# Kernel optimization log

Measured on AMD Instinct MI355X. Metric: run time of the kernel, lower is better.

## Reference

```python
import jax, jax.numpy as jnp
import numpy as np

Nc, Nq = 100000, 20000
Fc, Fq = 300, 768
HID, H, L = 128, 4, 2
D = HID // H
OUT = 8
E = 400000
NT, ET = 2, 3


def setup_inputs() -> dict:
    key = jax.random.key(0)
    ks = jax.random.split(key, 24)
    def n(i, shape, s=1.0):
        return jax.random.normal(ks[i], shape, dtype=jnp.float32) * s
    return {
        'x_context': n(0, (Nc, Fc)),
        'x_question': n(1, (Nq, Fq)),
        'src_q2c': jax.random.randint(ks[2], (E,), 0, Nq),
        'dst_q2c': jax.random.randint(ks[3], (E,), 0, Nc),
        'src_c2c': jax.random.randint(ks[4], (E,), 0, Nc),
        'dst_c2c': jax.random.randint(ks[5], (E,), 0, Nc),
        'src_c2q': jax.random.randint(ks[6], (E,), 0, Nc),
        'dst_c2q': jax.random.randint(ks[7], (E,), 0, Nq),
        'in_W_context': n(8, (Fc, HID), 0.05),
        'in_b_context': jnp.zeros((HID,), jnp.float32),
        'in_W_question': n(9, (Fq, HID), 0.05),
        'in_b_question': jnp.zeros((HID,), jnp.float32),
        'k_W': n(10, (L, NT, HID, HID), 0.05),
        'k_b': jnp.zeros((L, NT, HID), jnp.float32),
        'q_W': n(11, (L, NT, HID, HID), 0.05),
        'q_b': jnp.zeros((L, NT, HID), jnp.float32),
        'v_W': n(12, (L, NT, HID, HID), 0.05),
        'v_b': jnp.zeros((L, NT, HID), jnp.float32),
        'a_W': n(13, (L, NT, HID, HID), 0.05),
        'a_b': jnp.zeros((L, NT, HID), jnp.float32),
        'skip': jnp.ones((L, NT), jnp.float32),
        'a_rel': n(14, (L, ET, H, D, D), 0.1),
        'm_rel': n(15, (L, ET, H, D, D), 0.1),
        'p_rel': jnp.ones((L, ET, H), jnp.float32),
        'out_W': n(16, (HID, OUT), 0.05),
        'out_b': jnp.zeros((OUT,), jnp.float32),
    }


def segment_softmax(logits, seg, num):
    # logits: [E, H], seg: [E] destination node ids
    m = jax.ops.segment_max(logits, seg, num_segments=num)
    m = jnp.where(jnp.isfinite(m), m, 0.0)
    e = jnp.exp(logits - m[seg])
    s = jax.ops.segment_sum(e, seg, num_segments=num)
    return e / (s[seg] + 1e-16)


def reference(x_context, x_question, src_q2c, dst_q2c, src_c2c, dst_c2c,
              src_c2q, dst_c2q, in_W_context, in_b_context, in_W_question,
              in_b_question, k_W, k_b, q_W, q_b, v_W, v_b, a_W, a_b, skip,
              a_rel, m_rel, p_rel, out_W, out_b):
    # node type 0 = 'context', 1 = 'question'
    x = [jax.nn.relu(x_context @ in_W_context + in_b_context),
         jax.nn.relu(x_question @ in_W_question + in_b_question)]
    Ns = [x[0].shape[0], x[1].shape[0]]
    # (src_nt, dst_nt, src_idx, dst_idx) per edge type
    edge_types = [(1, 0, src_q2c, dst_q2c),
                  (0, 0, src_c2c, dst_c2c),
                  (0, 1, src_c2q, dst_c2q)]
    scale = 1.0 / jnp.sqrt(jnp.float32(D))
    for l in range(L):
        k = [(x[nt] @ k_W[l, nt] + k_b[l, nt]).reshape(-1, H, D) for nt in range(NT)]
        q = [(x[nt] @ q_W[l, nt] + q_b[l, nt]).reshape(-1, H, D) for nt in range(NT)]
        v = [(x[nt] @ v_W[l, nt] + v_b[l, nt]).reshape(-1, H, D) for nt in range(NT)]
        agg = [jnp.zeros((Ns[nt], H, D), x[0].dtype) for nt in range(NT)]
        for et, (snt, dnt, src, dst) in enumerate(edge_types):
            k_rel = jnp.einsum('ehd,hdf->ehf', k[snt][src], a_rel[l, et])
            v_rel = jnp.einsum('ehd,hdf->ehf', v[snt][src], m_rel[l, et])
            logits = jnp.einsum('ehd,ehd->eh', q[dnt][dst], k_rel) * p_rel[l, et] * scale
            alpha = segment_softmax(logits, dst, Ns[dnt])  # [E, H]
            agg[dnt] = agg[dnt].at[dst].add(v_rel * alpha[:, :, None])
        for nt in range(NT):
            o = jax.nn.gelu(agg[nt].reshape(Ns[nt], HID), approximate=False)
            o = o @ a_W[l, nt] + a_b[l, nt]
            g = jax.nn.sigmoid(skip[l, nt])
            x[nt] = g * o + (1.0 - g) * x[nt]
    return x[0] @ out_W + out_b
```

## Files before the change

kernel.cpp:

```cpp
#include <hip/hip_runtime.h>

constexpr int NC = 100000;
constexpr int NQ = 20000;
constexpr int FC = 300;
constexpr int FQ = 768;
constexpr int NEDGE = 400000;
constexpr int NTOT = NC + NC + NQ;
constexpr int NTOT2 = NC + NQ;
constexpr int NB0 = (NC + 127) / 128;
constexpr int NB1 = (NQ + 127) / 128;
constexpr int NBALL = NB0 + NB1;
constexpr int NBC64 = (NC + 63) / 64;
constexpr int NBQ64 = (NQ + 63) / 64;
constexpr int NBALL64 = NBC64 + NBQ64;
constexpr float SCALE = 0.17677669529663687f;
constexpr float LOG2E = 1.4426950408889634f;

typedef __attribute__((ext_vector_type(8))) short bf16x8;
typedef __attribute__((ext_vector_type(4))) float f32x4;
typedef unsigned short u16;

__device__ __forceinline__ float gelu_f(float x) {
  return 0.5f * x * (1.0f + erff(x * 0.7071067811865476f));
}
__device__ __forceinline__ u16 bf16_rne(float x) {
  unsigned u = __float_as_uint(x);
  unsigned r = u + 0x7fffu + ((u >> 16) & 1u);
  return (u16)(r >> 16);
}
__device__ __forceinline__ float bf16_to_f(u16 h) {
  return __uint_as_float(((unsigned)h) << 16);
}
__device__ __forceinline__ void split2(float x, u16& hi, u16& lo) {
  hi = bf16_rne(x);
  lo = bf16_rne(x - bf16_to_f(hi));
}
__device__ __forceinline__ void splitT(float x, u16& hi, u16& lo) {
  hi = (u16)(__float_as_uint(x) >> 16);
  lo = bf16_rne(x - bf16_to_f(hi));
}

__global__ void k_count3(const int* __restrict__ d0, const int* __restrict__ d1,
                         const int* __restrict__ d2, int* __restrict__ counts) {
  int i = blockIdx.x * 256 + threadIdx.x;
  if (i >= 3 * NEDGE) return;
  int et = i / NEDGE, e = i - et * NEDGE;
  int d = (et == 0) ? d0[e] : (et == 1) ? d1[e] : d2[e];
  int base = (et == 0) ? 0 : (et == 1) ? NC : 2 * NC;
  atomicAdd(&counts[base + d], 1);
}

__global__ void k_scan_block(const int* __restrict__ in, int* __restrict__ out,
                             int* __restrict__ bsum, int n) {
  __shared__ int s[256];
  int tid = threadIdx.x;
  int i = blockIdx.x * 256 + tid;
  int v = (i < n) ? in[i] : 0;
  s[tid] = v;
  __syncthreads();
  for (int off = 1; off < 256; off <<= 1) {
    int t = (tid >= off) ? s[tid - off] : 0;
    __syncthreads();
    s[tid] += t;
    __syncthreads();
  }
  if (i < n) out[i] = s[tid] - v;
  if (tid == 255) bsum[blockIdx.x] = s[255];
}

__global__ void k_scan_sums(int* __restrict__ bsum, int nb) {
  __shared__ int s[1024];
  int tid = threadIdx.x;
  int v = (tid < nb) ? bsum[tid] : 0;
  s[tid] = v;
  __syncthreads();
  for (int off = 1; off < 1024; off <<= 1) {
    int t = (tid >= off) ? s[tid - off] : 0;
    __syncthreads();
    s[tid] += t;
    __syncthreads();
  }
  if (tid < nb) bsum[tid] = s[tid] - v;
}

__global__ void k_scan_add(int* __restrict__ ptr, const int* __restrict__ bsum,
                           int* __restrict__ cursor, int n, int total) {
  int i = blockIdx.x * 256 + threadIdx.x;
  if (i < n) {
    int v = ptr[i] + bsum[blockIdx.x];
    ptr[i] = v;
    cursor[i] = v;
  }
  if (i == 0) ptr[n] = total;
}

__global__ void k_scatter3(const int* __restrict__ s0, const int* __restrict__ s1,
                           const int* __restrict__ s2, const int* __restrict__ d0,
                           const int* __restrict__ d1, const int* __restrict__ d2,
                           int* __restrict__ cursor, int* __restrict__ srcs_out) {
  int i = blockIdx.x * 256 + threadIdx.x;
  if (i >= 3 * NEDGE) return;
  int et = i / NEDGE, e = i - et * NEDGE;
  int d = (et == 0) ? d0[e] : (et == 1) ? d1[e] : d2[e];
  int sv = (et == 0) ? s0[e] : (et == 1) ? s1[e] : s2[e];
  int base = (et == 0) ? 0 : (et == 1) ? NC : 2 * NC;
  int p = atomicAdd(&cursor[base + d], 1);
  srcs_out[p] = sv;
}

__global__ void prep_all(const float* __restrict__ kW, const float* __restrict__ kB,
                         const float* __restrict__ qW, const float* __restrict__ qB,
                         const float* __restrict__ vW, const float* __restrict__ vB,
                         const float* __restrict__ aW, const float* __restrict__ aB,
                         const float* __restrict__ arel, const float* __restrict__ mrel,
                         const float* __restrict__ prel,
                         u16* __restrict__ Bth, u16* __restrict__ Btl,
                         float* __restrict__ biasOut) {
  int i = blockIdx.x;
  int col = threadIdx.x;
  int y = blockIdx.y;
  int l = y / 10, yy = y % 10;
  size_t lw = (size_t)l * 2 * 16384, lb = (size_t)l * 2 * 128;
  size_t le = (size_t)l * 3 * 4096, lp = (size_t)l * 3 * 4;
  const float *W = nullptr, *bb = nullptr, *rel = nullptr, *pr = nullptr;
  float mscale = 1.0f;
  bool fold = false;
  switch (yy) {
    case 0: W = qW + lw; bb = qB + lb; break;
    case 1: fold = true; W = kW + lw; bb = kB + lb; rel = arel + le + 4096; pr = prel + lp + 4; mscale = SCALE; break;
    case 2: fold = true; W = vW + lw; bb = vB + lb; rel = mrel + le + 4096; break;
    case 3: fold = true; W = kW + lw; bb = kB + lb; rel = arel + le + 8192; pr = prel + lp + 8; mscale = SCALE; break;
    case 4: fold = true; W = vW + lw; bb = vB + lb; rel = mrel + le + 8192; break;
    case 5: W = qW + lw + 16384; bb = qB + lb + 128; break;
    case 6: fold = true; W = kW + lw + 16384; bb = kB + lb + 128; rel = arel + le; pr = prel + lp; mscale = SCALE; break;
    case 7: fold = true; W = vW + lw + 16384; bb = vB + lb + 128; rel = mrel + le; break;
    case 8: W = aW + lw; bb = aB + lb; break;
    default: W = aW + lw + 16384; bb = aB + lb + 128; break;
  }
  int colOff = y * 128;
  if (!fold) {
    float v = W[i * 128 + col];
    u16 hi, lo;
    split2(v, hi, lo);
    Bth[(size_t)(colOff + col) * 128 + i] = hi;
    Btl[(size_t)(colOff + col) * 128 + i] = lo;
    if (i == 0) biasOut[colOff + col] = bb[col];
    return;
  }
  int h = col >> 5, f = col & 31;
  float m = (pr ? pr[h] : 1.0f) * mscale;
  float s = 0.0f;
  #pragma unroll
  for (int d = 0; d < 32; ++d)
    s += W[i * 128 + h * 32 + d] * rel[(h * 32 + d) * 32 + f];
  s *= m;
  u16 hi, lo;
  split2(s, hi, lo);
  Bth[(size_t)(colOff + col) * 128 + i] = hi;
  Btl[(size_t)(colOff + col) * 128 + i] = lo;
  if (i == 0) {
    float sb = 0.0f;
    #pragma unroll
    for (int d = 0; d < 32; ++d)
      sb += bb[h * 32 + d] * rel[(h * 32 + d) * 32 + f];
    biasOut[colOff + col] = sb * m;
  }
}

__global__ void split_in(const float* __restrict__ Wc, const float* __restrict__ bc,
                         const float* __restrict__ Wq, const float* __restrict__ bq,
                         u16* __restrict__ Bth, u16* __restrict__ Btl,
                         float* __restrict__ biasOut) {
  int n = blockIdx.x, y = blockIdx.y;
  const float* W = y ? Wq : Wc;
  const float* b = y ? bq : bc;
  int K = y ? FQ : FC, Kp = y ? 768 : 320;
  size_t boff = y ? (size_t)128 * 320 : 0;
  for (int k = threadIdx.x; k < Kp; k += 256) {
    float v = (k < K) ? W[(size_t)k * 128 + n] : 0.0f;
    u16 hi, lo;
    split2(v, hi, lo);
    Bth[boff + (size_t)n * Kp + k] = hi;
    Btl[boff + (size_t)n * Kp + k] = lo;
  }
  if (threadIdx.x == 0) biasOut[(y ? 128 : 0) + n] = b[n];
}

template <int MODE>
__global__ __launch_bounds__(256) void pipe_gemm(
    const float* __restrict__ Ac, const float* __restrict__ Aq,
    const u16* __restrict__ Bth, const u16* __restrict__ Btl,
    const float* __restrict__ biasBuf,
    u16* __restrict__ xh_all, u16* __restrict__ xl_all,
    const float* __restrict__ skip, int l) {
  __shared__ u16 smem[15360];
  constexpr int AH = 0, AL = 2560, BH = 5120, BL = 10240;
  const int tid = threadIdx.x, lane = tid & 63, wv = tid >> 6;
  const int l15 = lane & 15, g4 = lane >> 4, koff = g4 * 8;
  const int srA = tid >> 2, scA = (tid & 3) * 8;
  const int srB = tid >> 1, scB = (tid & 1) * 16;

  const int bid = blockIdx.x;
  const int nt = (bid < NBC64) ? 0 : 1;
  const int m0 = nt ? (bid - NBC64) * 64 : bid * 64;
  const int M = nt ? NQ : NC;
  const int rowbase = nt ? NC : 0;
  const float* A32;
  int K, Kp, biasOff;
  size_t boff, arow;
  if (MODE == 1) {
    if (nt == 0) { A32 = Ac; K = FC; Kp = 320; boff = 0; biasOff = 0; }
    else { A32 = Aq; K = FQ; Kp = 768; boff = (size_t)128 * 320; biasOff = 128; }
    arow = (size_t)(m0 + srA) * K;
  } else {
    A32 = Ac;
    K = 128; Kp = 128;
    boff = (size_t)(8 + nt) * 16384;
    biasOff = (8 + nt) * 128;
    arow = (size_t)(rowbase + m0 + srA) * 128;
  }
  const bool rowokA = (m0 + srA) < M;
  const int nk = (K + 31) / 32;

  f32x4 acc[8];
  #pragma unroll
  for (int ni = 0; ni < 8; ++ni) acc[ni] = (f32x4){0.f, 0.f, 0.f, 0.f};

  auto loadA = [&](float va[8], int k0) {
    if (rowokA && (k0 + 32 <= K)) {
      const float* ap = A32 + arow + k0 + scA;
      float4 f0 = *(const float4*)ap;
      float4 f1 = *(const float4*)(ap + 4);
      va[0] = f0.x; va[1] = f0.y; va[2] = f0.z; va[3] = f0.w;
      va[4] = f1.x; va[5] = f1.y; va[6] = f1.z; va[7] = f1.w;
    } else {
      #pragma unroll
      for (int j = 0; j < 8; ++j) {
        int kc = k0 + scA + j;
        va[j] = (rowokA && kc < K) ? A32[arow + kc] : 0.0f;
      }
    }
  };
  auto loadB = [&](uint4& bh0, uint4& bh1, uint4& bl0, uint4& bl1, int k0) {
    const u16* bp = Bth + boff + (size_t)srB * Kp + k0 + scB;
    bh0 = *(const uint4*)bp;
    bh1 = *(const uint4*)(bp + 8);
    const u16* lp = Btl + boff + (size_t)srB * Kp + k0 + scB;
    bl0 = *(const uint4*)lp;
    bl1 = *(const uint4*)(lp + 8);
  };

  float vaC[8];
  uint4 bhC0, bhC1, blC0, blC1;
  loadA(vaC, 0);
  loadB(bhC0, bhC1, blC0, blC1, 0);

  for (int ks = 0; ks < nk; ++ks) {
    {
      alignas(16) u16 hv[8], lv[8];
      #pragma unroll
      for (int j = 0; j < 8; ++j) {
        float x = (MODE == 2) ? gelu_f(vaC[j]) : vaC[j];
        splitT(x, hv[j], lv[j]);
      }
      *(uint4*)&smem[AH + srA * 40 + scA] = *(const uint4*)hv;
      *(uint4*)&smem[AL + srA * 40 + scA] = *(const uint4*)lv;
      *(uint4*)&smem[BH + srB * 40 + scB] = bhC0;
      *(uint4*)&smem[BH + srB * 40 + scB + 8] = bhC1;
      *(uint4*)&smem[BL + srB * 40 + scB] = blC0;
      *(uint4*)&smem[BL + srB * 40 + scB + 8] = blC1;
    }
    __syncthreads();

    float vaN[8];
    uint4 bhN0, bhN1, blN0, blN1;
    const bool more = (ks + 1) < nk;
    if (more) {
      loadA(vaN, (ks + 1) * 32);
      loadB(bhN0, bhN1, blN0, blN1, (ks + 1) * 32);
    }

    {
      int row = wv * 16 + l15;
      bf16x8 a_h = *(const bf16x8*)&smem[AH + row * 40 + koff];
      bf16x8 a_l = *(const bf16x8*)&smem[AL + row * 40 + koff];
      #pragma unroll
      for (int ni = 0; ni < 8; ++ni) {
        int col = ni * 16 + l15;
        bf16x8 b_h = *(const bf16x8*)&smem[BH + col * 40 + koff];
        bf16x8 b_l = *(const bf16x8*)&smem[BL + col * 40 + koff];
        acc[ni] = __builtin_amdgcn_mfma_f32_16x16x32_bf16(a_h, b_h, acc[ni], 0, 0, 0);
        acc[ni] = __builtin_amdgcn_mfma_f32_16x16x32_bf16(a_l, b_h, acc[ni], 0, 0, 0);
        acc[ni] = __builtin_amdgcn_mfma_f32_16x16x32_bf16(a_h, b_l, acc[ni], 0, 0, 0);
      }
    }
    __syncthreads();

    if (more) {
      #pragma unroll
      for (int j = 0; j < 8; ++j) vaC[j] = vaN[j];
      bhC0 = bhN0; bhC1 = bhN1; blC0 = blN0; blC1 = blN1;
    }
  }

  float g = 1.0f;
  if (MODE == 2) g = 1.0f / (1.0f + __expf(-skip[l * 2 + nt]));

  const int rl0 = wv * 16 + g4 * 4;
  #pragma unroll
  for (int ni = 0; ni < 8; ++ni) {
    int colL = ni * 16 + l15;
    float bi = biasBuf[biasOff + colL];
    #pragma unroll
    for (int rr = 0; rr < 4; ++rr) {
      int row = m0 + rl0 + rr;
      float o = acc[ni][rr] + bi;
      if (MODE == 1) {
        o = fmaxf(o, 0.0f);
      } else if (row < M) {
        size_t idx = (size_t)(rowbase + row) * 128 + colL;
        float xo = bf16_to_f(xh_all[idx]) + bf16_to_f(xl_all[idx]);
        o = g * o + (1.0f - g) * xo;
      }
      acc[ni][rr] = o;
    }
  }

  const int wrow = tid >> 2, wseg = tid & 3;
  #pragma unroll
  for (int ph = 0; ph < 2; ++ph) {
    if (ph) __syncthreads();
    #pragma unroll
    for (int ni = 0; ni < 8; ++ni) {
      #pragma unroll
      for (int rr = 0; rr < 4; ++rr) {
        u16 hh, ll;
        split2(acc[ni][rr], hh, ll);
        smem[(rl0 + rr) * 136 + ni * 16 + l15] = ph ? ll : hh;
      }
    }
    __syncthreads();
    int grow = m0 + wrow;
    if (grow < M) {
      u16* dstp = ph ? xl_all : xh_all;
      uint4* dst = (uint4*)&dstp[(size_t)(rowbase + grow) * 128 + wseg * 32];
      const uint4* src = (const uint4*)&smem[wrow * 136 + wseg * 32];
      #pragma unroll
      for (int j = 0; j < 4; ++j) dst[j] = src[j];
    }
  }
}

__global__ __launch_bounds__(256) void proj_all(
    const u16* __restrict__ xh_all,
    const u16* __restrict__ Bth, const float* __restrict__ biasBuf,
    u16* __restrict__ q_all, u16* __restrict__ kvA,
    u16* __restrict__ kvB1, u16* __restrict__ kvB2) {
  int bid = blockIdx.x, y = blockIdx.y;
  int nt = (bid < NB0) ? 0 : 1;
  if (nt == 1 && y >= 3) return;
  __shared__ u16 smem[10240];
  constexpr int AH = 0, BH = 5120;
  int m0 = nt ? (bid - NB0) * 128 : bid * 128;
  int M = nt ? NQ : NC;
  int abase = nt ? NC : 0;
  int bslab = nt ? 5 + y : y;
  u16* cp; int ld, cb, crowbase;
  if (nt == 0) {
    switch (y) {
      case 0: cp = q_all; ld = 128; cb = 0; crowbase = 0; break;
      case 1: cp = kvB1; ld = 256; cb = 0; crowbase = 0; break;
      case 2: cp = kvB1; ld = 256; cb = 128; crowbase = 0; break;
      case 3: cp = kvB2; ld = 256; cb = 0; crowbase = 0; break;
      default: cp = kvB2; ld = 256; cb = 128; crowbase = 0; break;
    }
  } else {
    switch (y) {
      case 0: cp = q_all; ld = 128; cb = 0; crowbase = NC; break;
      case 1: cp = kvA; ld = 256; cb = 0; crowbase = 0; break;
      default: cp = kvA; ld = 256; cb = 128; crowbase = 0; break;
    }
  }
  const int tid = threadIdx.x, lane = tid & 63, wv = tid >> 6;
  const int l15 = lane & 15, g4 = lane >> 4, koff = g4 * 8;
  const int sr = tid >> 1, sc = (tid & 1) * 16;
  const bool rowok = (m0 + sr) < M;

  f32x4 acc[2][8];
  #pragma unroll
  for (int mi = 0; mi < 2; ++mi)
    #pragma unroll
    for (int ni = 0; ni < 8; ++ni) acc[mi][ni] = (f32x4){0.f, 0.f, 0.f, 0.f};

  for (int k0 = 0; k0 < 128; k0 += 32) {
    uint4 h0 = {0, 0, 0, 0}, h1 = {0, 0, 0, 0};
    if (rowok) {
      const u16* ap = xh_all + (size_t)(abase + m0 + sr) * 128 + k0 + sc;
      h0 = *(const uint4*)ap;
      h1 = *(const uint4*)(ap + 8);
    }
    *(uint4*)&smem[AH + sr * 40 + sc] = h0;
    *(uint4*)&smem[AH + sr * 40 + sc + 8] = h1;
    {
      const u16* bp = Bth + (size_t)(bslab * 128 + sr) * 128 + k0 + sc;
      *(uint4*)&smem[BH + sr * 40 + sc] = *(const uint4*)bp;
      *(uint4*)&smem[BH + sr * 40 + sc + 8] = *(const uint4*)(bp + 8);
    }
    __syncthreads();

    bf16x8 a_h[2];
    #pragma unroll
    for (int mi = 0; mi < 2; ++mi) {
      int row = wv * 32 + mi * 16 + l15;
      a_h[mi] = *(const bf16x8*)&smem[AH + row * 40 + koff];
    }
    #pragma unroll
    for (int ni = 0; ni < 8; ++ni) {
      int col = ni * 16 + l15;
      bf16x8 b_h = *(const bf16x8*)&smem[BH + col * 40 + koff];
      #pragma unroll
      for (int mi = 0; mi < 2; ++mi)
        acc[mi][ni] = __builtin_amdgcn_mfma_f32_16x16x32_bf16(a_h[mi], b_h, acc[mi][ni], 0, 0, 0);
    }
    __syncthreads();
  }

  const int wrow = tid >> 2, wseg = tid & 3;
  #pragma unroll
  for (int h = 0; h < 2; ++h) {
    if (h) __syncthreads();
    if ((wv >> 1) == h) {
      #pragma unroll
      for (int mi = 0; mi < 2; ++mi) {
        int rl = (wv & 1) * 32 + mi * 16 + g4 * 4;
        #pragma unroll
        for (int ni = 0; ni < 8; ++ni) {
          float bi = biasBuf[bslab * 128 + ni * 16 + l15];
          #pragma unroll
          for (int rr = 0; rr < 4; ++rr)
            smem[(rl + rr) * 136 + ni * 16 + l15] = bf16_rne(acc[mi][ni][rr] + bi);
        }
      }
    }
    __syncthreads();
    int grow = m0 + h * 64 + wrow;
    if (grow < M) {
      uint4* dst = (uint4*)&cp[(size_t)(crowbase + grow) * ld + cb + wseg * 32];
      const uint4* src = (const uint4*)&smem[wrow * 136 + wseg * 32];
      #pragma unroll
      for (int j = 0; j < 4; ++j) dst[j] = src[j];
    }
  }
}

__device__ __forceinline__ void attn_seg(
    const u16* __restrict__ kv, int start, int end,
    const int* __restrict__ srcs, const float q8[8], int lane, float accO[8]) {
  if (start >= end) return;
  float sum = 0.0f;
  float acc[8];
  #pragma unroll
  for (int i = 0; i < 8; ++i) acc[i] = 0.0f;
  const int half = lane >> 5;
  const int sub = lane & 31;
  const int bsrc = lane & 44;
  #pragma unroll 2
  for (int e = start; e < end; e += 2) {
    int ee = e + half;
    bool valid = ee < end;
    int cl = valid ? ee : end - 1;
    int s = srcs[cl];
    uint4 u = *(const uint4*)&kv[(size_t)s * 256 + sub * 8];
    float r[8];
    r[0] = bf16_to_f((u16)(u.x & 0xffffu)); r[1] = bf16_to_f((u16)(u.x >> 16));
    r[2] = bf16_to_f((u16)(u.y & 0xffffu)); r[3] = bf16_to_f((u16)(u.y >> 16));
    r[4] = bf16_to_f((u16)(u.z & 0xffffu)); r[5] = bf16_to_f((u16)(u.z >> 16));
    r[6] = bf16_to_f((u16)(u.w & 0xffffu)); r[7] = bf16_to_f((u16)(u.w >> 16));
    float p = q8[0] * r[0];
    #pragma unroll
    for (int i = 1; i < 8; ++i) p = fmaf(q8[i], r[i], p);
    p += __shfl_xor(p, 1);
    p += __shfl_xor(p, 2);
    p = fminf(p, 100.0f);
    float w = valid ? exp2f(p) : 0.0f;
    float wB = __shfl(w, bsrc);
    sum += wB;
    #pragma unroll
    for (int i = 0; i < 8; ++i) acc[i] = fmaf(wB, r[i], acc[i]);
  }
  sum += __shfl_xor(sum, 32);
  #pragma unroll
  for (int i = 0; i < 8; ++i) acc[i] += __shfl_xor(acc[i], 32);
  float inv = 1.0f / (sum + 1e-16f);
  #pragma unroll
  for (int i = 0; i < 8; ++i) accO[i] = fmaf(acc[i], inv, accO[i]);
}

__global__ __launch_bounds__(256) void attn_all(
    const u16* __restrict__ q_all, const u16* __restrict__ kvA,
    const u16* __restrict__ kvB1, const u16* __restrict__ kvB2,
    const int* __restrict__ ptr_all, const int* __restrict__ srcs_all,
    float* __restrict__ agg_all) {
  int wave = threadIdx.x >> 6, lane = threadIdx.x & 63;
  int node = blockIdx.x * 4 + wave;
  if (node >= NTOT2) return;
  int sub = lane & 31;
  float q8[8];
  #pragma unroll
  for (int i = 0; i < 8; ++i) q8[i] = 0.0f;
  if (sub < 16) {
    uint4 u = *(const uint4*)&q_all[(size_t)node * 128 + sub * 8];
    q8[0] = bf16_to_f((u16)(u.x & 0xffffu)) * LOG2E; q8[1] = bf16_to_f((u16)(u.x >> 16)) * LOG2E;
    q8[2] = bf16_to_f((u16)(u.y & 0xffffu)) * LOG2E; q8[3] = bf16_to_f((u16)(u.y >> 16)) * LOG2E;
    q8[4] = bf16_to_f((u16)(u.z & 0xffffu)) * LOG2E; q8[5] = bf16_to_f((u16)(u.z >> 16)) * LOG2E;
    q8[6] = bf16_to_f((u16)(u.w & 0xffffu)) * LOG2E; q8[7] = bf16_to_f((u16)(u.w >> 16)) * LOG2E;
  }
  float accO[8];
  #pragma unroll
  for (int i = 0; i < 8; ++i) accO[i] = 0.0f;
  if (node < NC) {
    attn_seg(kvA, ptr_all[node], ptr_all[node + 1], srcs_all, q8, lane, accO);
    attn_seg(kvB1, ptr_all[NC + node], ptr_all[NC + node + 1], srcs_all, q8, lane, accO);
  } else {
    int idx = 2 * NC + (node - NC);
    attn_seg(kvB2, ptr_all[idx], ptr_all[idx + 1], srcs_all, q8, lane, accO);
  }
  if (lane >= 16 && lane < 32) {
    int j = lane - 16;
    float4 o0 = {accO[0], accO[1], accO[2], accO[3]};
    float4 o1 = {accO[4], accO[5], accO[6], accO[7]};
    *(float4*)&agg_all[(size_t)node * 128 + j * 8] = o0;
    *(float4*)&agg_all[(size_t)node * 128 + j * 8 + 4] = o1;
  }
}

__global__ __launch_bounds__(256) void gemm_out(const u16* __restrict__ Xh,
                                                const u16* __restrict__ Xl,
                                                const float* __restrict__ W,
                                                const float* __restrict__ b,
                                                float* __restrict__ out, int M) {
  __shared__ float Ws[1024];
  __shared__ float As[32][129];
  int tid = threadIdx.x;
  int m0 = blockIdx.x * 32;
  *(float4*)&Ws[tid * 4] = *(const float4*)&W[tid * 4];
  {
    int r = tid >> 3;
    int c0 = (tid & 7) * 16;
    if (m0 + r < M) {
      const u16* hp = Xh + (size_t)(m0 + r) * 128 + c0;
      const u16* lp = Xl + (size_t)(m0 + r) * 128 + c0;
      #pragma unroll
      for (int j = 0; j < 16; ++j) As[r][c0 + j] = bf16_to_f(hp[j]) + bf16_to_f(lp[j]);
    } else {
      #pragma unroll
      for (int j = 0; j < 16; ++j) As[r][c0 + j] = 0.0f;
    }
  }
  __syncthreads();
  int r = tid >> 3, c = tid & 7;
  float sum = b[c];
  #pragma unroll 16
  for (int k = 0; k < 128; ++k) sum = fmaf(As[r][k], Ws[k * 8 + c], sum);
  if (m0 + r < M) out[(size_t)(m0 + r) * 8 + c] = sum;
}

static inline size_t align256(size_t x) { return (x + 255) & ~(size_t)255; }

extern "C" void kernel_launch(void* const* d_in, const int* in_sizes, int n_in,
                              void* d_out, int out_size, void* d_ws, size_t ws_size,
                              hipStream_t stream) {
  const float* x_context = (const float*)d_in[0];
  const float* x_question = (const float*)d_in[1];
  const int* src_q2c = (const int*)d_in[2];
  const int* dst_q2c = (const int*)d_in[3];
  const int* src_c2c = (const int*)d_in[4];
  const int* dst_c2c = (const int*)d_in[5];
  const int* src_c2q = (const int*)d_in[6];
  const int* dst_c2q = (const int*)d_in[7];
  const float* inWc = (const float*)d_in[8];
  const float* inbc = (const float*)d_in[9];
  const float* inWq = (const float*)d_in[10];
  const float* inbq = (const float*)d_in[11];
  const float* kW = (const float*)d_in[12];
  const float* kB = (const float*)d_in[13];
  const float* qW = (const float*)d_in[14];
  const float* qB = (const float*)d_in[15];
  const float* vW = (const float*)d_in[16];
  const float* vB = (const float*)d_in[17];
  const float* aW = (const float*)d_in[18];
  const float* aB = (const float*)d_in[19];
  const float* skip = (const float*)d_in[20];
  const float* arel = (const float*)d_in[21];
  const float* mrel = (const float*)d_in[22];
  const float* prel = (const float*)d_in[23];
  const float* outW = (const float*)d_in[24];
  const float* outb = (const float*)d_in[25];

  char* base = (char*)d_ws;
  size_t off = 0;
  auto carve = [&](size_t bytes) -> void* {
    void* p = base + off;
    off = align256(off + bytes);
    return p;
  };
  u16* xh_all = (u16*)carve((size_t)NTOT2 * 128 * 2);
  u16* xl_all = (u16*)carve((size_t)NTOT2 * 128 * 2);
  u16* q_all = (u16*)carve((size_t)NTOT2 * 128 * 2);
  u16* kvA = (u16*)carve((size_t)NQ * 256 * 2);
  u16* kvB1 = (u16*)carve((size_t)NC * 256 * 2);
  u16* kvB2 = (u16*)carve((size_t)NC * 256 * 2);
  float* agg_all = (float*)carve((size_t)NTOT2 * 128 * 4);
  u16* Bth = (u16*)carve((size_t)2560 * 128 * 2);
  u16* Btl = (u16*)carve((size_t)2560 * 128 * 2);
  u16* BthI = (u16*)carve((size_t)(320 + 768) * 128 * 2);
  u16* BtlI = (u16*)carve((size_t)(320 + 768) * 128 * 2);
  float* biasBuf = (float*)carve(2560 * 4);
  float* biasIn = (float*)carve(256 * 4);
  int* ptr_all = (int*)carve((size_t)(NTOT + 1) * 4);
  int* srcs_all = (int*)carve((size_t)3 * NEDGE * 4);
  int* counts = (int*)carve((size_t)NTOT * 4);
  int* cursor = (int*)carve((size_t)NTOT * 4);
  int* blksums = (int*)carve(2048 * 4);

  {
    int nb = (NTOT + 255) / 256;
    hipMemsetAsync(counts, 0, (size_t)NTOT * 4, stream);
    k_count3<<<(3 * NEDGE + 255) / 256, 256, 0, stream>>>(dst_q2c, dst_c2c, dst_c2q, counts);
    k_scan_block<<<nb, 256, 0, stream>>>(counts, ptr_all, blksums, NTOT);
    k_scan_sums<<<1, 1024, 0, stream>>>(blksums, nb);
    k_scan_add<<<nb, 256, 0, stream>>>(ptr_all, blksums, cursor, NTOT, 3 * NEDGE);
    k_scatter3<<<(3 * NEDGE + 255) / 256, 256, 0, stream>>>(
        src_q2c, src_c2c, src_c2q, dst_q2c, dst_c2c, dst_c2q, cursor, srcs_all);
  }

  split_in<<<dim3(128, 2), 256, 0, stream>>>(inWc, inbc, inWq, inbq, BthI, BtlI, biasIn);
  prep_all<<<dim3(128, 20), 128, 0, stream>>>(kW, kB, qW, qB, vW, vB, aW, aB,
                                              arel, mrel, prel, Bth, Btl, biasBuf);

  pipe_gemm<1><<<NBALL64, 256, 0, stream>>>(x_context, x_question, BthI, BtlI, biasIn,
                                            xh_all, xl_all, nullptr, 0);

  for (int l = 0; l < 2; ++l) {
    const u16* BthL = Bth + (size_t)l * 10 * 128 * 128;
    const u16* BtlL = Btl + (size_t)l * 10 * 128 * 128;
    const float* biasL = biasBuf + (size_t)l * 1280;
    proj_all<<<dim3(NBALL, 5), 256, 0, stream>>>(xh_all, BthL, biasL,
                                                 q_all, kvA, kvB1, kvB2);
    attn_all<<<(NTOT2 + 3) / 4, 256, 0, stream>>>(q_all, kvA, kvB1, kvB2,
                                                  ptr_all, srcs_all, agg_all);
    pipe_gemm<2><<<NBALL64, 256, 0, stream>>>(agg_all, nullptr, BthL, BtlL, biasL,
                                              xh_all, xl_all, skip, l);
  }

  gemm_out<<<(NC + 31) / 32, 256, 0, stream>>>(xh_all, xl_all, outW, outb, (float*)d_out, NC);
}
```

Measured before the change: 796.0 us.

## Skip dead question-node work in last layer and unroll attention edge loop

In the final layer only context outputs feed the readout, so question-node attention, its update GEMM, and the projections that only feed those nodes (context K/V for c2q, question Q) are skipped. The attention segment loop now handles two edge pairs per iteration with independent loads, so more gathers are in flight. The dead-code elimination is legitimate because question features after layer 2 are never used. The risk is mis-indexed skip conditions in proj_all, plus higher register pressure in the attention loop.

Result: faster. 696.2 us (-12.5%).

```diff
diff --git a/kernel.cpp b/kernel.cpp
--- a/kernel.cpp
+++ b/kernel.cpp
@@ -355,10 +355,14 @@
     const u16* __restrict__ xh_all,
     const u16* __restrict__ Bth, const float* __restrict__ biasBuf,
     u16* __restrict__ q_all, u16* __restrict__ kvA,
-    u16* __restrict__ kvB1, u16* __restrict__ kvB2) {
+    u16* __restrict__ kvB1, u16* __restrict__ kvB2, int last) {
   int bid = blockIdx.x, y = blockIdx.y;
   int nt = (bid < NB0) ? 0 : 1;
   if (nt == 1 && y >= 3) return;
+  if (last) {
+    if (nt == 0 && y >= 3) return;
+    if (nt == 1 && y == 0) return;
+  }
   __shared__ u16 smem[10240];
   constexpr int AH = 0, BH = 5120;
   int m0 = nt ? (bid - NB0) * 128 : bid * 128;
@@ -464,29 +468,48 @@
   const int half = lane >> 5;
   const int sub = lane & 31;
   const int bsrc = lane & 44;
-  #pragma unroll 2
-  for (int e = start; e < end; e += 2) {
-    int ee = e + half;
-    bool valid = ee < end;
-    int cl = valid ? ee : end - 1;
-    int s = srcs[cl];
-    uint4 u = *(const uint4*)&kv[(size_t)s * 256 + sub * 8];
-    float r[8];
-    r[0] = bf16_to_f((u16)(u.x & 0xffffu)); r[1] = bf16_to_f((u16)(u.x >> 16));
-    r[2] = bf16_to_f((u16)(u.y & 0xffffu)); r[3] = bf16_to_f((u16)(u.y >> 16));
-    r[4] = bf16_to_f((u16)(u.z & 0xffffu)); r[5] = bf16_to_f((u16)(u.z >> 16));
-    r[6] = bf16_to_f((u16)(u.w & 0xffffu)); r[7] = bf16_to_f((u16)(u.w >> 16));
-    float p = q8[0] * r[0];
-    #pragma unroll
-    for (int i = 1; i < 8; ++i) p = fmaf(q8[i], r[i], p);
-    p += __shfl_xor(p, 1);
-    p += __shfl_xor(p, 2);
-    p = fminf(p, 100.0f);
-    float w = valid ? exp2f(p) : 0.0f;
-    float wB = __shfl(w, bsrc);
-    sum += wB;
-    #pragma unroll
-    for (int i = 0; i < 8; ++i) acc[i] = fmaf(wB, r[i], acc[i]);
+  for (int e = start; e < end; e += 4) {
+    int e0 = e + half;
+    int e1 = e + 2 + half;
+    bool v0 = e0 < end, v1 = e1 < end;
+    int c0 = v0 ? e0 : end - 1;
+    int c1 = v1 ? e1 : end - 1;
+    int s0 = srcs[c0];
+    int s1 = srcs[c1];
+    uint4 u0 = *(const uint4*)&kv[(size_t)s0 * 256 + sub * 8];
+    uint4 u1 = *(const uint4*)&kv[(size_t)s1 * 256 + sub * 8];
+    float r0[8], r1[8];
+    r0[0] = bf16_to_f((u16)(u0.x & 0xffffu)); r0[1] = bf16_to_f((u16)(u0.x >> 16));
+    r0[2] = bf16_to_f((u16)(u0.y & 0xffffu)); r0[3] = bf16_to_f((u16)(u0.y >> 16));
+    r0[4] = bf16_to_f((u16)(u0.z & 0xffffu)); r0[5] = bf16_to_f((u16)(u0.z >> 16));
+    r0[6] = bf16_to_f((u16)(u0.w & 0xffffu)); r0[7] = bf16_to_f((u16)(u0.w >> 16));
+    r1[0] = bf16_to_f((u16)(u1.x & 0xffffu)); r1[1] = bf16_to_f((u16)(u1.x >> 16));
+    r1[2] = bf16_to_f((u16)(u1.y & 0xffffu)); r1[3] = bf16_to_f((u16)(u1.y >> 16));
+    r1[4] = bf16_to_f((u16)(u1.z & 0xffffu)); r1[5] = bf16_to_f((u16)(u1.z >> 16));
+    r1[6] = bf16_to_f((u16)(u1.w & 0xffffu)); r1[7] = bf16_to_f((u16)(u1.w >> 16));
+    float p0 = q8[0] * r0[0];
+    float p1 = q8[0] * r1[0];
+    #pragma unroll
+    for (int i = 1; i < 8; ++i) {
+      p0 = fmaf(q8[i], r0[i], p0);
+      p1 = fmaf(q8[i], r1[i], p1);
+    }
+    p0 += __shfl_xor(p0, 1);
+    p1 += __shfl_xor(p1, 1);
+    p0 += __shfl_xor(p0, 2);
+    p1 += __shfl_xor(p1, 2);
+    p0 = fminf(p0, 100.0f);
+    p1 = fminf(p1, 100.0f);
+    float w0 = v0 ? exp2f(p0) : 0.0f;
+    float w1 = v1 ? exp2f(p1) : 0.0f;
+    float wB0 = __shfl(w0, bsrc);
+    float wB1 = __shfl(w1, bsrc);
+    sum += wB0 + wB1;
+    #pragma unroll
+    for (int i = 0; i < 8; ++i) {
+      acc[i] = fmaf(wB0, r0[i], acc[i]);
+      acc[i] = fmaf(wB1, r1[i], acc[i]);
+    }
   }
   sum += __shfl_xor(sum, 32);
   #pragma unroll
@@ -500,10 +523,10 @@
     const u16* __restrict__ q_all, const u16* __restrict__ kvA,
     const u16* __restrict__ kvB1, const u16* __restrict__ kvB2,
     const int* __restrict__ ptr_all, const int* __restrict__ srcs_all,
-    float* __restrict__ agg_all) {
+    float* __restrict__ agg_all, int ncap) {
   int wave = threadIdx.x >> 6, lane = threadIdx.x & 63;
   int node = blockIdx.x * 4 + wave;
-  if (node >= NTOT2) return;
+  if (node >= ncap) return;
   int sub = lane & 31;
   float q8[8];
   #pragma unroll
@@ -642,15 +665,17 @@
                                             xh_all, xl_all, nullptr, 0);
 
   for (int l = 0; l < 2; ++l) {
+    const int last = (l == 1);
     const u16* BthL = Bth + (size_t)l * 10 * 128 * 128;
     const u16* BtlL = Btl + (size_t)l * 10 * 128 * 128;
     const float* biasL = biasBuf + (size_t)l * 1280;
     proj_all<<<dim3(NBALL, 5), 256, 0, stream>>>(xh_all, BthL, biasL,
-                                                 q_all, kvA, kvB1, kvB2);
-    attn_all<<<(NTOT2 + 3) / 4, 256, 0, stream>>>(q_all, kvA, kvB1, kvB2,
-                                                  ptr_all, srcs_all, agg_all);
-    pipe_gemm<2><<<NBALL64, 256, 0, stream>>>(agg_all, nullptr, BthL, BtlL, biasL,
-                                              xh_all, xl_all, skip, l);
+                                                 q_all, kvA, kvB1, kvB2, last);
+    int ncap = last ? NC : NTOT2;
+    attn_all<<<(ncap + 3) / 4, 256, 0, stream>>>(q_all, kvA, kvB1, kvB2,
+                                                 ptr_all, srcs_all, agg_all, ncap);
+    pipe_gemm<2><<<last ? NBC64 : NBALL64, 256, 0, stream>>>(agg_all, nullptr, BthL, BtlL, biasL,
+                                                             xh_all, xl_all, skip, l);
   }
 
   gemm_out<<<(NC + 31) / 32, 256, 0, stream>>>(xh_all, xl_all, outW, outb, (float*)d_out, NC);
```
